# Performance work log

Hardware: AMD Instinct MI355X
Metric: run time of the kernel (lower is better)

## Reference

```python
import jax, jax.numpy as jnp
import numpy as np

B, L, H, A, M, E, R = 4, 1024, 1024, 16, 128, 32, 992
EMB, BLK, C = 768, 64, 97


def setup_inputs() -> dict:
    key = jax.random.key(0)
    ks = jax.random.split(key, 8)
    return {
        'seq_lhs': jax.random.normal(ks[0], (B, L, H), jnp.float32),
        'ent_lhs': jax.random.normal(ks[1], (B, M, H), jnp.float32),
        'ent_to_seq_attn': jax.random.uniform(ks[2], (B, A, M, L), jnp.float32),
        'mention_entity_ids': jax.random.randint(ks[3], (B, M), 0, E, jnp.int32),
        'hts': jax.random.randint(ks[4], (B, R, 2), 0, E, jnp.int32),
        'head_W': jax.random.normal(ks[5], (2 * H, EMB), jnp.float32) * 0.02,
        'head_b': jnp.zeros((EMB,), jnp.float32),
        'tail_W': jax.random.normal(ks[6], (2 * H, EMB), jnp.float32) * 0.02,
        'tail_b': jnp.zeros((EMB,), jnp.float32),
        'bil_W': jax.random.normal(ks[7], (EMB * BLK, C), jnp.float32) * 0.02,
        'bil_b': jnp.zeros((C,), jnp.float32),
    }


def _pool_doc(seq, ents, attn, ids, ht):
    # seq [L,H], ents [M,H], attn [A,M,L], ids [M], ht [R,2]
    counts = jax.ops.segment_sum(jnp.ones((M,), seq.dtype), ids, num_segments=E)  # [E]
    nz = counts > 0
    # stable segment logsumexp over mentions of each entity (matches torch.logsumexp;
    # single-mention entities reduce to the raw embedding, empty entities -> zeros)
    mx = jax.ops.segment_max(ents, ids, num_segments=E)              # [E,H]
    mx = jnp.where(nz[:, None], mx, 0.0)
    s = jax.ops.segment_sum(jnp.exp(ents - mx[ids]), ids, num_segments=E)
    s = jnp.where(nz[:, None], s, 1.0)
    ent_emb = jnp.where(nz[:, None], mx + jnp.log(s), 0.0)           # [E,H]
    # mean of mention->seq attention per entity (empty -> zeros)
    attn_m = jnp.transpose(attn, (1, 0, 2))                          # [M,A,L]
    asum = jax.ops.segment_sum(attn_m, ids, num_segments=E)          # [E,A,L]
    ent_attn = jnp.where(nz[:, None, None], asum / jnp.maximum(counts, 1.0)[:, None, None], 0.0)
    # gather head/tail entities for each pair
    hs, ts = ent_emb[ht[:, 0]], ent_emb[ht[:, 1]]                    # [R,H]
    ha, ta = ent_attn[ht[:, 0]], ent_attn[ht[:, 1]]                  # [R,A,L]
    w = (ha * ta).mean(axis=1)                                       # [R,L]
    w = w / (w.sum(axis=1, keepdims=True) + 1e-5)
    rel = jnp.einsum('ld,rl->rd', seq, w)                            # [R,H]
    return hs, ts, rel


def reference(seq_lhs, ent_lhs, ent_to_seq_attn, mention_entity_ids, hts,
              head_W, head_b, tail_W, tail_b, bil_W, bil_b):
    hs, ts, rel = jax.vmap(_pool_doc)(seq_lhs, ent_lhs, ent_to_seq_attn,
                                      mention_entity_ids, hts)
    hs = hs.reshape(-1, H)
    ts = ts.reshape(-1, H)
    rel = rel.reshape(-1, H)
    hs = jnp.tanh(jnp.concatenate([hs, rel], axis=1) @ head_W + head_b)  # [N,EMB]
    ts = jnp.tanh(jnp.concatenate([ts, rel], axis=1) @ tail_W + tail_b)
    b1 = hs.reshape(-1, EMB // BLK, BLK)
    b2 = ts.reshape(-1, EMB // BLK, BLK)
    bl = (b1[:, :, :, None] * b2[:, :, None, :]).reshape(-1, EMB * BLK)  # [N,EMB*BLK]
    return bl @ bil_W + bil_b                                            # [N,C]
```

## Files before the change

### kernel.cpp

```cpp
#include <hip/hip_runtime.h>
#include <hip/hip_bf16.h>
#include <math.h>

constexpr int cB   = 4;
constexpr int cL   = 1024;
constexpr int cH   = 1024;
constexpr int cA   = 16;
constexpr int cM   = 128;
constexpr int cE   = 32;
constexpr int cR   = 992;
constexpr int cEMB = 768;
constexpr int cC   = 97;
constexpr int cN   = cB * cR;
constexpr int cNG  = 8;

typedef unsigned short ushort;
typedef __attribute__((ext_vector_type(4))) unsigned short ushort4v;
typedef __attribute__((ext_vector_type(8))) short short8;
typedef __attribute__((ext_vector_type(4))) float float4v;

static __device__ inline float bf2f(ushort u) {
    unsigned v = ((unsigned)u) << 16;
    float f;
    __builtin_memcpy(&f, &v, 4);
    return f;
}
static __device__ inline ushort f2bf(float f) {
    unsigned u;
    __builtin_memcpy(&u, &f, 4);
    unsigned r = (u + 0x7FFFu + ((u >> 16) & 1u)) >> 16;
    return (ushort)r;
}

static __device__ inline void gld16(const ushort* src, ushort* dstbase) {
    __builtin_amdgcn_global_load_lds(
        (const __attribute__((address_space(1))) unsigned int*)src,
        (__attribute__((address_space(3))) unsigned int*)dstbase, 16, 0, 0);
}

__global__ void tr_bf16_k(const float* __restrict__ src, ushort* __restrict__ dst,
                          int R, int C, int Cp) {
    int z = blockIdx.z;
    int r0 = blockIdx.x * 32, c0 = blockIdx.y * 32;
    int tx = threadIdx.x & 31, ty = threadIdx.x >> 5;
    __shared__ float tile[32][33];
    for (int p = 0; p < 4; p++) {
        int r = r0 + ty + p * 8, c = c0 + tx;
        tile[ty + p * 8][tx] = (r < R && c < C) ? src[((size_t)z * R + r) * C + c] : 0.f;
    }
    __syncthreads();
    for (int p = 0; p < 4; p++) {
        int c = c0 + ty + p * 8, r = r0 + tx;
        if (c < Cp && r < R)
            dst[((size_t)z * Cp + c) * R + r] = f2bf(tile[tx][ty + p * 8]);
    }
}

__global__ void tr_ht_k(const float* __restrict__ Wh, const float* __restrict__ Wt,
                        ushort* __restrict__ WTh, ushort* __restrict__ WTt) {
    const float* src = blockIdx.z ? Wt : Wh;
    ushort* dst = blockIdx.z ? WTt : WTh;
    int r0 = blockIdx.x * 32, c0 = blockIdx.y * 32;
    int tx = threadIdx.x & 31, ty = threadIdx.x >> 5;
    __shared__ float tile[32][33];
    for (int p = 0; p < 4; p++) {
        int r = r0 + ty + p * 8, c = c0 + tx;
        tile[ty + p * 8][tx] = src[(size_t)r * cEMB + c];
    }
    __syncthreads();
    for (int p = 0; p < 4; p++) {
        int c = c0 + ty + p * 8, r = r0 + tx;
        dst[(size_t)c * (2 * cH) + r] = f2bf(tile[tx][ty + p * 8]);
    }
}

__global__ void wf_build_k(const float* __restrict__ W, ushort* __restrict__ Wf) {
    const int si = blockIdx.x;
    const int tid = threadIdx.x;
    __shared__ ushort sWb[64 * 136];
    for (int idx = tid; idx < 64 * 128; idx += 256) {
        int r = idx >> 7, c = idx & 127;
        float v = (c < cC) ? W[((size_t)si * 64 + r) * cC + c] : 0.f;
        sWb[r * 136 + c] = f2bf(v);
    }
    __syncthreads();
#pragma unroll
    for (int p = 0; p < 4; p++) {
        int e = tid + p * 256;
        int f = e >> 6, lane = e & 63;
        int g = lane >> 4, col = lane & 15;
        int khalf = f >> 3, ct = f & 7;
        int jb = khalf * 32 + g * 8;
        int c = ct * 16 + col;
        short8 v;
#pragma unroll
        for (int jj = 0; jj < 8; jj++) v[jj] = (short)sWb[(jb + jj) * 136 + c];
        *(short8*)&Wf[(((size_t)si * 16 + f) * 64 + lane) * 8] = v;
    }
}

__global__ void ent_pool_k(const float* __restrict__ ent_lhs, const int* __restrict__ ids,
                           ushort* __restrict__ ent_emb, int* __restrict__ counts) {
    int e = blockIdx.x, b = blockIdx.y;
    __shared__ int sid[cM];
    int tid = threadIdx.x;
    if (tid < cM) sid[tid] = ids[b * cM + tid];
    __syncthreads();
    int cnt = 0;
    for (int m = 0; m < cM; m++) cnt += (sid[m] == e) ? 1 : 0;
    if (blockIdx.z == 0 && tid == 0) counts[b * cE + e] = cnt;
    int h = blockIdx.z * 256 + tid;
    {
        float mx = -1e30f;
        for (int m = 0; m < cM; m++)
            if (sid[m] == e) mx = fmaxf(mx, ent_lhs[(size_t)(b * cM + m) * cH + h]);
        float s = 0.f;
        for (int m = 0; m < cM; m++)
            if (sid[m] == e) s += __expf(ent_lhs[(size_t)(b * cM + m) * cH + h] - mx);
        ent_emb[(size_t)(b * cE + e) * cH + h] = f2bf((cnt > 0) ? (mx + __logf(s)) : 0.f);
    }
}

__global__ void ent_attn_k(const float* __restrict__ attn, const int* __restrict__ ids,
                           const int* __restrict__ counts, ushort* __restrict__ ent_attn) {
    int ba = blockIdx.x;
    int b = ba / cA, a = ba % cA;
    int tid = threadIdx.x;
    int l = blockIdx.y * 256 + tid;
    __shared__ int sid[cM];
    __shared__ int scnt[cE];
    __shared__ float sacc[256 * 33];
    if (tid < cM) sid[tid] = ids[b * cM + tid];
    if (tid < cE) scnt[tid] = counts[b * cE + tid];
    float* acc = &sacc[tid * 33];
    for (int e2 = 0; e2 < cE; e2++) acc[e2] = 0.f;
    __syncthreads();
    const float* ap = attn + ((size_t)(b * cA + a) * cM) * cL + l;
    for (int m = 0; m < cM; m++) acc[sid[m]] += ap[(size_t)m * cL];
    for (int e2 = 0; e2 < cE; e2++) {
        ent_attn[((size_t)(b * cE + e2) * cA + a) * cL + l] =
            f2bf(acc[e2] / (float)max(scnt[e2], 1));
    }
}

__global__ void w_k(const ushort* __restrict__ ent_attn, const int* __restrict__ hts,
                    ushort* __restrict__ w) {
    int nr = blockIdx.x;
    int b = nr / cR;
    int he = hts[nr * 2 + 0], te = hts[nr * 2 + 1];
    int tid = threadIdx.x;
    int l0 = tid * 4;
    const ushort* ha = ent_attn + ((size_t)(b * cE + he) * cA) * cL + l0;
    const ushort* ta = ent_attn + ((size_t)(b * cE + te) * cA) * cL + l0;
    float v[4] = {0.f, 0.f, 0.f, 0.f};
#pragma unroll
    for (int a = 0; a < cA; a++) {
        ushort4v hv = *(const ushort4v*)&ha[(size_t)a * cL];
        ushort4v tv = *(const ushort4v*)&ta[(size_t)a * cL];
#pragma unroll
        for (int i = 0; i < 4; i++) v[i] += bf2f(hv[i]) * bf2f(tv[i]);
    }
    float psum = 0.f;
#pragma unroll
    for (int i = 0; i < 4; i++) { v[i] *= (1.0f / cA); psum += v[i]; }
    for (int off = 32; off > 0; off >>= 1) psum += __shfl_down(psum, off, 64);
    __shared__ float red[4];
    if ((tid & 63) == 0) red[tid >> 6] = psum;
    __syncthreads();
    float tot = red[0] + red[1] + red[2] + red[3];
    float inv = 1.0f / (tot + 1e-5f);
    ushort4v o;
#pragma unroll
    for (int i = 0; i < 4; i++) o[i] = f2bf(v[i] * inv);
    *(ushort4v*)&w[(size_t)nr * cL + l0] = o;
}

__global__ __launch_bounds__(256) void
rel_mfma_k(const ushort* __restrict__ wbf, const ushort* __restrict__ seqT,
           ushort* __restrict__ relbf) {
    const int b = blockIdx.z;
    const int r0 = blockIdx.x * 128, h0 = blockIdx.y * 64;
    const int tid = threadIdx.x, lane = tid & 63, wv = tid >> 6;
    const int col = lane & 15, g = lane >> 4;

    __shared__ ushort sA[128 * 72];
    __shared__ ushort sB[64 * 72];

    float4v acc[2][4];
#pragma unroll
    for (int mt = 0; mt < 2; mt++)
#pragma unroll
        for (int ct = 0; ct < 4; ct++) acc[mt][ct] = (float4v){0.f, 0.f, 0.f, 0.f};

    for (int kt = 0; kt < cL; kt += 64) {
#pragma unroll
        for (int p = 0; p < 4; p++) {
            int t = tid + p * 256;
            int row = t >> 3, seg = t & 7;
            int r = min(r0 + row, cR - 1);
            *(short8*)&sA[row * 72 + seg * 8] =
                *(const short8*)&wbf[((size_t)b * cR + r) * cL + kt + seg * 8];
        }
#pragma unroll
        for (int p = 0; p < 2; p++) {
            int t = tid + p * 256;
            int c = t >> 3, seg = t & 7;
            *(short8*)&sB[c * 72 + seg * 8] =
                *(const short8*)&seqT[((size_t)b * cH + h0 + c) * cL + kt + seg * 8];
        }
        __syncthreads();
        const int wrow = wv * 32;
#pragma unroll
        for (int k0 = 0; k0 < 64; k0 += 32) {
            short8 a0 = *(const short8*)&sA[(wrow + col) * 72 + k0 + g * 8];
            short8 a1 = *(const short8*)&sA[(wrow + 16 + col) * 72 + k0 + g * 8];
#pragma unroll
            for (int ct = 0; ct < 4; ct++) {
                short8 bf = *(const short8*)&sB[(ct * 16 + col) * 72 + k0 + g * 8];
                acc[0][ct] = __builtin_amdgcn_mfma_f32_16x16x32_bf16(a0, bf, acc[0][ct], 0, 0, 0);
                acc[1][ct] = __builtin_amdgcn_mfma_f32_16x16x32_bf16(a1, bf, acc[1][ct], 0, 0, 0);
            }
        }
        __syncthreads();
    }
#pragma unroll
    for (int mt = 0; mt < 2; mt++) {
#pragma unroll
        for (int ct = 0; ct < 4; ct++) {
            int h = h0 + ct * 16 + col;
            int rowb = r0 + wv * 32 + mt * 16 + g * 4;
#pragma unroll
            for (int reg = 0; reg < 4; reg++) {
                int r = rowb + reg;
                if (r < cR)
                    relbf[((size_t)b * cR + r) * cH + h] = f2bf(acc[mt][ct][reg]);
            }
        }
    }
}

__global__ __launch_bounds__(256) void
proj_mfma2_k(const ushort* __restrict__ ent_bf, const ushort* __restrict__ relbf,
             const int* __restrict__ hts,
             const ushort* __restrict__ WTh, const ushort* __restrict__ WTt,
             const float* __restrict__ head_b, const float* __restrict__ tail_b,
             ushort* __restrict__ hsp, ushort* __restrict__ tsp) {
    const int sel = blockIdx.z;
    const ushort* WTp = sel ? WTt : WTh;
    const float* bias = sel ? tail_b : head_b;
    ushort* outp = sel ? tsp : hsp;

    const int e0 = blockIdx.x * 128, n0 = blockIdx.y * 64;
    const int tid = threadIdx.x, lane = tid & 63, wv = tid >> 6;
    const int col = lane & 15, g4 = lane >> 4;
    const int wr = wv >> 1, wc = wv & 1;

    __shared__ ushort sA[64 * 64];
    __shared__ ushort sB[128 * 64];

    const int lr = lane >> 3;
    const int swz = (lane & 7) ^ lr;

    const int ra0 = wv * 8 + lr, ra1 = ra0 + 32;
    size_t eb0, eb1;
    { int n = n0 + ra0, bb = n / cR; eb0 = ((size_t)(bb * cE + hts[n * 2 + sel])) * cH; }
    { int n = n0 + ra1, bb = n / cR; eb1 = ((size_t)(bb * cE + hts[n * 2 + sel])) * cH; }
    const ushort* aent0 = ent_bf + eb0 + swz * 8;
    const ushort* aent1 = ent_bf + eb1 + swz * 8;
    const ushort* arel0 = relbf + (size_t)(n0 + ra0) * cH + swz * 8;
    const ushort* arel1 = relbf + (size_t)(n0 + ra1) * cH + swz * 8;

    const ushort* bptr[4];
#pragma unroll
    for (int p = 0; p < 4; p++)
        bptr[p] = WTp + (size_t)(e0 + p * 32 + wv * 8 + lr) * (2 * cH) + swz * 8;

    float4v acc[2][4];
#pragma unroll
    for (int mt = 0; mt < 2; mt++)
#pragma unroll
        for (int ct = 0; ct < 4; ct++) acc[mt][ct] = (float4v){0.f, 0.f, 0.f, 0.f};

    for (int kt = 0; kt < 2 * cH; kt += 64) {
        const bool first = kt < cH;
        const ushort* a0 = first ? aent0 + kt : arel0 + (kt - cH);
        const ushort* a1 = first ? aent1 + kt : arel1 + (kt - cH);
        gld16(a0, &sA[(0 * 4 + wv) * 512]);
        gld16(a1, &sA[(1 * 4 + wv) * 512]);
#pragma unroll
        for (int p = 0; p < 4; p++)
            gld16(bptr[p] + kt, &sB[(p * 4 + wv) * 512]);
        __syncthreads();

#pragma unroll
        for (int k0 = 0; k0 < 64; k0 += 32) {
            short8 av[2];
#pragma unroll
            for (int mt = 0; mt < 2; mt++) {
                int ra = wr * 32 + mt * 16 + col;
                int sg = ((k0 >> 3) + g4) ^ (ra & 7);
                av[mt] = *(const short8*)&sA[ra * 64 + sg * 8];
            }
#pragma unroll
            for (int ct = 0; ct < 4; ct++) {
                int rb = wc * 64 + ct * 16 + col;
                int sg = ((k0 >> 3) + g4) ^ (rb & 7);
                short8 bv = *(const short8*)&sB[rb * 64 + sg * 8];
#pragma unroll
                for (int mt = 0; mt < 2; mt++)
                    acc[mt][ct] = __builtin_amdgcn_mfma_f32_16x16x32_bf16(
                        av[mt], bv, acc[mt][ct], 0, 0, 0);
            }
        }
        __syncthreads();
    }

#pragma unroll
    for (int mt = 0; mt < 2; mt++) {
#pragma unroll
        for (int ct = 0; ct < 4; ct++) {
            int e = e0 + wc * 64 + ct * 16 + col;
            float bv = bias[e];
            int rowb = n0 + wr * 32 + mt * 16 + g4 * 4;
#pragma unroll
            for (int reg = 0; reg < 4; reg++)
                outp[(size_t)(rowb + reg) * cEMB + e] = f2bf(tanhf(acc[mt][ct][reg] + bv));
        }
    }
}

__global__ __launch_bounds__(256) void
bil_mfma11_k(const ushort* __restrict__ hsp, const ushort* __restrict__ tsp,
             const ushort* __restrict__ Wf, float* __restrict__ part) {
    const int grp = blockIdx.x;
    const int n0 = blockIdx.y * 64;
    const int tid = threadIdx.x;
    const int lane = tid & 63, wv = tid >> 6;
    const int col = lane & 15, g4 = lane >> 4;

    __shared__ float sHs[32 * 68];

    float4v acc[4][2];
#pragma unroll
    for (int mt = 0; mt < 4; mt++)
#pragma unroll
        for (int ctl = 0; ctl < 2; ctl++) acc[mt][ctl] = (float4v){0.f, 0.f, 0.f, 0.f};

    const ushort* WfG = Wf + (size_t)grp * 3 * 32 * 8192;
    const ushort* wbase = WfG + ((size_t)(wv * 2) * 64 + lane) * 8;

#define WLOAD(dst, t) {                                                        \
        const ushort* _p = wbase + (size_t)(t) * 8192;                         \
        dst[0][0] = *(const short8*)&_p[0];                                    \
        dst[0][1] = *(const short8*)&_p[512];                                  \
        dst[1][0] = *(const short8*)&_p[4096];                                 \
        dst[1][1] = *(const short8*)&_p[4608];                                 \
    }

#define BILSTEP(ii, w) {                                                       \
        float4v hsv[4];                                                        \
        _Pragma("unroll")                                                      \
        for (int mt = 0; mt < 4; mt++)                                         \
            hsv[mt] = *(const float4v*)&sHs[(ii) * 68 + mt * 16 + g4 * 4];     \
        _Pragma("unroll")                                                      \
        for (int ctl = 0; ctl < 2; ctl++) {                                    \
            _Pragma("unroll")                                                  \
            for (int mt = 0; mt < 4; mt++) {                                   \
                float4v P = (float4v){0.f, 0.f, 0.f, 0.f};                     \
                P = __builtin_amdgcn_mfma_f32_16x16x32_bf16(tsA[mt][0], w[0][ctl], P, 0, 0, 0); \
                P = __builtin_amdgcn_mfma_f32_16x16x32_bf16(tsA[mt][1], w[1][ctl], P, 0, 0, 0); \
                acc[mt][ctl] += hsv[mt] * P;                                   \
            }                                                                  \
        }                                                                      \
    }

    short8 tsA[4][2];
    short8 wA[2][2], wB[2][2];
    WLOAD(wA, 0);

    for (int s = 0; s < 3; ++s) {
        const int islice = grp * 3 + s;
        const int kb = islice >> 1;

        __syncthreads();
        {
            int row = tid & 63, seg = tid >> 6;
            short8 v = *(const short8*)
                &hsp[(size_t)(n0 + row) * cEMB + islice * 32 + seg * 8];
#pragma unroll
            for (int jj = 0; jj < 8; jj++)
                sHs[(seg * 8 + jj) * 68 + row] = bf2f((ushort)v[jj]);
        }
#pragma unroll
        for (int mt = 0; mt < 4; mt++)
#pragma unroll
            for (int kh = 0; kh < 2; kh++)
                tsA[mt][kh] = *(const short8*)
                    &tsp[(size_t)(n0 + mt * 16 + col) * cEMB
                         + kb * 64 + kh * 32 + g4 * 8];
        __syncthreads();

        for (int i = 0; i < 32; i += 2) {
            const int t = s * 32 + i;
            WLOAD(wB, t + 1);
            BILSTEP(i, wA);
            if (t + 2 < 96) WLOAD(wA, t + 2);
            BILSTEP(i + 1, wB);
        }
    }
#undef WLOAD
#undef BILSTEP

    float* pbase = part + (size_t)grp * cN * 128;
#pragma unroll
    for (int mt = 0; mt < 4; mt++) {
#pragma unroll
        for (int ctl = 0; ctl < 2; ctl++) {
            int c = (wv * 2 + ctl) * 16 + col;
            int rowb = n0 + mt * 16 + g4 * 4;
#pragma unroll
            for (int reg = 0; reg < 4; reg++)
                pbase[(size_t)(rowb + reg) * 128 + c] = acc[mt][ctl][reg];
        }
    }
}

__global__ void bil_reduce_k(const float* __restrict__ part,
                             const float* __restrict__ bil_b,
                             float* __restrict__ out) {
    int n = blockIdx.x;
    int c = threadIdx.x;
    if (c >= cC) return;
    float s = bil_b[c];
#pragma unroll
    for (int g = 0; g < cNG; g++)
        s += part[((size_t)g * cN + n) * 128 + c];
    out[(size_t)n * cC + c] = s;
}

extern "C" void kernel_launch(void* const* d_in, const int* in_sizes, int n_in,
                              void* d_out, int out_size, void* d_ws, size_t ws_size,
                              hipStream_t stream) {
    const float* seq_lhs  = (const float*)d_in[0];
    const float* ent_lhs  = (const float*)d_in[1];
    const float* attn     = (const float*)d_in[2];
    const int*   ids      = (const int*)d_in[3];
    const int*   hts      = (const int*)d_in[4];
    const float* head_W   = (const float*)d_in[5];
    const float* head_b   = (const float*)d_in[6];
    const float* tail_W   = (const float*)d_in[7];
    const float* tail_b   = (const float*)d_in[8];
    const float* bil_W    = (const float*)d_in[9];
    const float* bil_b    = (const float*)d_in[10];
    float* out = (float*)d_out;

    char* ws = (char*)d_ws;
    int*    counts   = (int*)(ws + 0);
    ushort* ent_bf   = (ushort*)(ws + 512);
    ushort* ent_attn = (ushort*)(ws + 262656);
    ushort* wbuf     = (ushort*)(ws + 4456960);
    ushort* relbf    = (ushort*)(ws + 12583424);
    ushort* hsp      = (ushort*)(ws + 20709888);
    ushort* tsp      = (ushort*)(ws + 26804736);
    ushort* Wf       = (ushort*)(ws + 32899584);
    ushort* WTh      = (ushort*)(ws + 45482496);
    ushort* WTt      = (ushort*)(ws + 48628224);
    ushort* seqT     = (ushort*)(ws + 51773952);
    float*  part     = (float*)(ws + 262656);

    hipLaunchKernelGGL(wf_build_k, dim3(768), dim3(256), 0, stream, bil_W, Wf);
    hipLaunchKernelGGL(tr_ht_k, dim3(64, 24, 2), dim3(256), 0, stream,
                       head_W, tail_W, WTh, WTt);
    hipLaunchKernelGGL(tr_bf16_k, dim3(32, 32, cB), dim3(256), 0, stream,
                       seq_lhs, seqT, cL, cH, cH);

    hipLaunchKernelGGL(ent_pool_k, dim3(cE, cB, 4), dim3(256), 0, stream,
                       ent_lhs, ids, ent_bf, counts);
    hipLaunchKernelGGL(ent_attn_k, dim3(cB * cA, cL / 256), dim3(256), 0, stream,
                       attn, ids, counts, ent_attn);
    hipLaunchKernelGGL(w_k, dim3(cN), dim3(256), 0, stream,
                       ent_attn, hts, wbuf);
    hipLaunchKernelGGL(rel_mfma_k, dim3(8, 16, cB), dim3(256), 0, stream,
                       wbuf, seqT, relbf);
    hipLaunchKernelGGL(proj_mfma2_k, dim3(cEMB / 128, cN / 64, 2), dim3(256), 0, stream,
                       ent_bf, relbf, hts, WTh, WTt, head_b, tail_b, hsp, tsp);
    hipLaunchKernelGGL(bil_mfma11_k, dim3(cNG, cN / 64), dim3(256), 0, stream,
                       hsp, tsp, Wf, part);
    hipLaunchKernelGGL(bil_reduce_k, dim3(cN), dim3(128), 0, stream,
                       part, bil_b, out);
}
```

Baseline: 322.5 us.

## Double-buffer LDS tiles in rel and proj GEMMs, raise MFMA priority in bilinear

The rel GEMM kernel is restructured to use direct global-to-LDS async loads with an XOR swizzle. Its tile is changed to 64 rows by 128 hidden columns on a 2x2 wave grid, and the next K tile is prefetched into a second LDS buffer while the current one is computed. The projection kernel gets the same double-buffering, so one barrier per iteration replaces the previous load-then-compute pair. The bilinear kernel wraps its MFMA section in s_setprio to favour matrix issue. The cost is twice the LDS per block, which may lower occupancy.

```diff
diff --git a/kernel.cpp b/kernel.cpp
--- a/kernel.cpp
+++ b/kernel.cpp
@@ -176,15 +176,27 @@
 }
 
 __global__ __launch_bounds__(256) void
-rel_mfma_k(const ushort* __restrict__ wbf, const ushort* __restrict__ seqT,
-           ushort* __restrict__ relbf) {
+rel_mfma2_k(const ushort* __restrict__ wbf, const ushort* __restrict__ seqT,
+            ushort* __restrict__ relbf) {
     const int b = blockIdx.z;
-    const int r0 = blockIdx.x * 128, h0 = blockIdx.y * 64;
+    const int h0 = blockIdx.x * 128, r0 = blockIdx.y * 64;
     const int tid = threadIdx.x, lane = tid & 63, wv = tid >> 6;
-    const int col = lane & 15, g = lane >> 4;
-
-    __shared__ ushort sA[128 * 72];
-    __shared__ ushort sB[64 * 72];
+    const int col = lane & 15, g4 = lane >> 4;
+    const int wr = wv >> 1, wc = wv & 1;
+
+    __shared__ ushort sA[2][64 * 64];
+    __shared__ ushort sB[2][128 * 64];
+
+    const int lr = lane >> 3;
+    const int swz = (lane & 7) ^ lr;
+
+    const int ra0 = wv * 8 + lr, ra1 = ra0 + 32;
+    const ushort* a0p = wbf + ((size_t)b * cR + min(r0 + ra0, cR - 1)) * cL + swz * 8;
+    const ushort* a1p = wbf + ((size_t)b * cR + min(r0 + ra1, cR - 1)) * cL + swz * 8;
+    const ushort* bptr[4];
+#pragma unroll
+    for (int p = 0; p < 4; p++)
+        bptr[p] = seqT + ((size_t)b * cH + h0 + p * 32 + wv * 8 + lr) * cL + swz * 8;
 
     float4v acc[2][4];
 #pragma unroll
@@ -192,43 +204,50 @@
 #pragma unroll
         for (int ct = 0; ct < 4; ct++) acc[mt][ct] = (float4v){0.f, 0.f, 0.f, 0.f};
 
+#define REL_STAGE(kt, buf) {                                                   \
+        gld16(a0p + (kt), &sA[buf][wv * 512]);                                 \
+        gld16(a1p + (kt), &sA[buf][(4 + wv) * 512]);                           \
+        _Pragma("unroll")                                                      \
+        for (int p = 0; p < 4; p++)                                            \
+            gld16(bptr[p] + (kt), &sB[buf][(p * 4 + wv) * 512]);               \
+    }
+
+    REL_STAGE(0, 0);
+    __syncthreads();
+    int cur = 0;
     for (int kt = 0; kt < cL; kt += 64) {
-#pragma unroll
-        for (int p = 0; p < 4; p++) {
-            int t = tid + p * 256;
-            int row = t >> 3, seg = t & 7;
-            int r = min(r0 + row, cR - 1);
-            *(short8*)&sA[row * 72 + seg * 8] =
-                *(const short8*)&wbf[((size_t)b * cR + r) * cL + kt + seg * 8];
-        }
-#pragma unroll
-        for (int p = 0; p < 2; p++) {
-            int t = tid + p * 256;
-            int c = t >> 3, seg = t & 7;
-            *(short8*)&sB[c * 72 + seg * 8] =
-                *(const short8*)&seqT[((size_t)b * cH + h0 + c) * cL + kt + seg * 8];
+        if (kt + 64 < cL) REL_STAGE(kt + 64, cur ^ 1);
+#pragma unroll
+        for (int k0 = 0; k0 < 64; k0 += 32) {
+            short8 av[2];
+#pragma unroll
+            for (int mt = 0; mt < 2; mt++) {
+                int ra = wr * 32 + mt * 16 + col;
+                int sg = ((k0 >> 3) + g4) ^ (ra & 7);
+                av[mt] = *(const short8*)&sA[cur][ra * 64 + sg * 8];
+            }
+#pragma unroll
+            for (int ct = 0; ct < 4; ct++) {
+                int rb = wc * 64 + ct * 16 + col;
+                int sg = ((k0 >> 3) + g4) ^ (rb & 7);
+                short8 bv = *(const short8*)&sB[cur][rb * 64 + sg * 8];
+#pragma unroll
+                for (int mt = 0; mt < 2; mt++)
+                    acc[mt][ct] = __builtin_amdgcn_mfma_f32_16x16x32_bf16(
+                        av[mt], bv, acc[mt][ct], 0, 0, 0);
+            }
         }
         __syncthreads();
-        const int wrow = wv * 32;
-#pragma unroll
-        for (int k0 = 0; k0 < 64; k0 += 32) {
-            short8 a0 = *(const short8*)&sA[(wrow + col) * 72 + k0 + g * 8];
-            short8 a1 = *(const short8*)&sA[(wrow + 16 + col) * 72 + k0 + g * 8];
-#pragma unroll
-            for (int ct = 0; ct < 4; ct++) {
-                short8 bf = *(const short8*)&sB[(ct * 16 + col) * 72 + k0 + g * 8];
-                acc[0][ct] = __builtin_amdgcn_mfma_f32_16x16x32_bf16(a0, bf, acc[0][ct], 0, 0, 0);
-                acc[1][ct] = __builtin_amdgcn_mfma_f32_16x16x32_bf16(a1, bf, acc[1][ct], 0, 0, 0);
-            }
-        }
-        __syncthreads();
-    }
+        cur ^= 1;
+    }
+#undef REL_STAGE
+
 #pragma unroll
     for (int mt = 0; mt < 2; mt++) {
 #pragma unroll
         for (int ct = 0; ct < 4; ct++) {
-            int h = h0 + ct * 16 + col;
-            int rowb = r0 + wv * 32 + mt * 16 + g * 4;
+            int h = h0 + wc * 64 + ct * 16 + col;
+            int rowb = r0 + wr * 32 + mt * 16 + g4 * 4;
 #pragma unroll
             for (int reg = 0; reg < 4; reg++) {
                 int r = rowb + reg;
@@ -240,7 +259,7 @@
 }
 
 __global__ __launch_bounds__(256) void
-proj_mfma2_k(const ushort* __restrict__ ent_bf, const ushort* __restrict__ relbf,
+proj_mfma3_k(const ushort* __restrict__ ent_bf, const ushort* __restrict__ relbf,
              const int* __restrict__ hts,
              const ushort* __restrict__ WTh, const ushort* __restrict__ WTt,
              const float* __restrict__ head_b, const float* __restrict__ tail_b,
@@ -255,8 +274,8 @@
     const int col = lane & 15, g4 = lane >> 4;
     const int wr = wv >> 1, wc = wv & 1;
 
-    __shared__ ushort sA[64 * 64];
-    __shared__ ushort sB[128 * 64];
+    __shared__ ushort sA[2][64 * 64];
+    __shared__ ushort sB[2][128 * 64];
 
     const int lr = lane >> 3;
     const int swz = (lane & 7) ^ lr;
@@ -281,17 +300,21 @@
 #pragma unroll
         for (int ct = 0; ct < 4; ct++) acc[mt][ct] = (float4v){0.f, 0.f, 0.f, 0.f};
 
+#define PROJ_STAGE(kt, buf) {                                                  \
+        const ushort* a0 = ((kt) < cH) ? aent0 + (kt) : arel0 + ((kt) - cH);   \
+        const ushort* a1 = ((kt) < cH) ? aent1 + (kt) : arel1 + ((kt) - cH);   \
+        gld16(a0, &sA[buf][wv * 512]);                                         \
+        gld16(a1, &sA[buf][(4 + wv) * 512]);                                   \
+        _Pragma("unroll")                                                      \
+        for (int p = 0; p < 4; p++)                                            \
+            gld16(bptr[p] + (kt), &sB[buf][(p * 4 + wv) * 512]);               \
+    }
+
+    PROJ_STAGE(0, 0);
+    __syncthreads();
+    int cur = 0;
     for (int kt = 0; kt < 2 * cH; kt += 64) {
-        const bool first = kt < cH;
-        const ushort* a0 = first ? aent0 + kt : arel0 + (kt - cH);
-        const ushort* a1 = first ? aent1 + kt : arel1 + (kt - cH);
-        gld16(a0, &sA[(0 * 4 + wv) * 512]);
-        gld16(a1, &sA[(1 * 4 + wv) * 512]);
-#pragma unroll
-        for (int p = 0; p < 4; p++)
-            gld16(bptr[p] + kt, &sB[(p * 4 + wv) * 512]);
-        __syncthreads();
-
+        if (kt + 64 < 2 * cH) PROJ_STAGE(kt + 64, cur ^ 1);
 #pragma unroll
         for (int k0 = 0; k0 < 64; k0 += 32) {
             short8 av[2];
@@ -299,13 +322,13 @@
             for (int mt = 0; mt < 2; mt++) {
                 int ra = wr * 32 + mt * 16 + col;
                 int sg = ((k0 >> 3) + g4) ^ (ra & 7);
-                av[mt] = *(const short8*)&sA[ra * 64 + sg * 8];
+                av[mt] = *(const short8*)&sA[cur][ra * 64 + sg * 8];
             }
 #pragma unroll
             for (int ct = 0; ct < 4; ct++) {
                 int rb = wc * 64 + ct * 16 + col;
                 int sg = ((k0 >> 3) + g4) ^ (rb & 7);
-                short8 bv = *(const short8*)&sB[rb * 64 + sg * 8];
+                short8 bv = *(const short8*)&sB[cur][rb * 64 + sg * 8];
 #pragma unroll
                 for (int mt = 0; mt < 2; mt++)
                     acc[mt][ct] = __builtin_amdgcn_mfma_f32_16x16x32_bf16(
@@ -313,7 +336,9 @@
             }
         }
         __syncthreads();
-    }
+        cur ^= 1;
+    }
+#undef PROJ_STAGE
 
 #pragma unroll
     for (int mt = 0; mt < 2; mt++) {
@@ -362,6 +387,7 @@
         _Pragma("unroll")                                                      \
         for (int mt = 0; mt < 4; mt++)                                         \
             hsv[mt] = *(const float4v*)&sHs[(ii) * 68 + mt * 16 + g4 * 4];     \
+        __builtin_amdgcn_s_setprio(1);                                         \
         _Pragma("unroll")                                                      \
         for (int ctl = 0; ctl < 2; ctl++) {                                    \
             _Pragma("unroll")                                                  \
@@ -372,6 +398,7 @@
                 acc[mt][ctl] += hsv[mt] * P;                                   \
             }                                                                  \
         }                                                                      \
+        __builtin_amdgcn_s_setprio(0);                                         \
     }
 
     short8 tsA[4][2];
@@ -480,9 +507,9 @@
                        attn, ids, counts, ent_attn);
     hipLaunchKernelGGL(w_k, dim3(cN), dim3(256), 0, stream,
                        ent_attn, hts, wbuf);
-    hipLaunchKernelGGL(rel_mfma_k, dim3(8, 16, cB), dim3(256), 0, stream,
+    hipLaunchKernelGGL(rel_mfma2_k, dim3(cH / 128, 16, cB), dim3(256), 0, stream,
                        wbuf, seqT, relbf);
-    hipLaunchKernelGGL(proj_mfma2_k, dim3(cEMB / 128, cN / 64, 2), dim3(256), 0, stream,
+    hipLaunchKernelGGL(proj_mfma3_k, dim3(cEMB / 128, cN / 64, 2), dim3(256), 0, stream,
                        ent_bf, relbf, hts, WTh, WTt, head_b, tail_b, hsp, tsp);
     hipLaunchKernelGGL(bil_mfma11_k, dim3(cNG, cN / 64), dim3(256), 0, stream,
                        hsp, tsp, Wf, part);
```

Result: faster. 312.6 us (-3.1%).
